# Optimization experiments

Measured on AMD Instinct MI355X. Metric: run time of the kernel, lower is better.

Reference implementation:

```python
import jax, jax.numpy as jnp
import numpy as np

N = 50000       # nodes
E = 800000      # edges (before self-loops)
F_IN = 128
HID = 64
HEADS = 4
OUT_DIM = 128
N_CLS = 2
NG = 500        # num graphs
SLOPE = 0.2     # GATConv leaky_relu negative slope
EPS = 1e-5      # BatchNorm eps


def setup_inputs() -> dict:
    key = jax.random.key(0)
    ks = jax.random.split(key, 24)
    s = 0.05
    d = {
        "x": jax.random.normal(ks[0], (N, F_IN), jnp.float32),
        "edge_index": jax.random.randint(ks[1], (2, E), 0, N, jnp.int64),
        "batch": jnp.sort(jax.random.randint(ks[2], (N,), 0, NG, jnp.int64)),
        # GATConv 1
        "W1": jax.random.normal(ks[3], (F_IN, HEADS * HID), jnp.float32) * s,
        "att_src1": jax.random.normal(ks[4], (HEADS, HID), jnp.float32) * s,
        "att_dst1": jax.random.normal(ks[5], (HEADS, HID), jnp.float32) * s,
        "b1": jnp.zeros((HEADS * HID,), jnp.float32),
        # BN1 (eval mode)
        "g1": jnp.ones((HEADS * HID,), jnp.float32),
        "be1": jnp.zeros((HEADS * HID,), jnp.float32),
        "rm1": jnp.zeros((HEADS * HID,), jnp.float32),
        "rv1": jnp.ones((HEADS * HID,), jnp.float32),
        # GATConv 2
        "W2": jax.random.normal(ks[6], (HEADS * HID, HEADS * HID), jnp.float32) * s,
        "att_src2": jax.random.normal(ks[7], (HEADS, HID), jnp.float32) * s,
        "att_dst2": jax.random.normal(ks[8], (HEADS, HID), jnp.float32) * s,
        "b2": jnp.zeros((HEADS * HID,), jnp.float32),
        # BN2 (eval mode)
        "g2": jnp.ones((HEADS * HID,), jnp.float32),
        "be2": jnp.zeros((HEADS * HID,), jnp.float32),
        "rm2": jnp.zeros((HEADS * HID,), jnp.float32),
        "rv2": jnp.ones((HEADS * HID,), jnp.float32),
        # MLP head
        "lw1": jax.random.normal(ks[9], (HEADS * HID, OUT_DIM), jnp.float32) * s,
        "lb1": jnp.zeros((OUT_DIM,), jnp.float32),
        "lw2": jax.random.normal(ks[10], (OUT_DIM, N_CLS), jnp.float32) * s,
        "lb2": jnp.zeros((N_CLS,), jnp.float32),
    }
    return d


def _gat_conv(x, src, dst, W, a_src, a_dst, b):
    """PyG GATConv (concat heads, add_self_loops=True, eval -> no dropout)."""
    n = x.shape[0]
    h = (x @ W).reshape(n, HEADS, -1)            # [N, H, C]
    loop = jnp.arange(n)
    s = jnp.concatenate([src, loop])             # self-loops appended
    d = jnp.concatenate([dst, loop])
    a_s = jnp.sum(h * a_src, axis=-1)            # [N, H]
    a_d = jnp.sum(h * a_dst, axis=-1)            # [N, H]
    e = jax.nn.leaky_relu(a_s[s] + a_d[d], SLOPE)   # [Et, H]
    # softmax over incoming edges per destination node
    m = jax.ops.segment_max(e, d, num_segments=n)
    ex = jnp.exp(e - m[d])
    denom = jax.ops.segment_sum(ex, d, num_segments=n)
    alpha = ex / denom[d]                        # [Et, H]
    msg = h[s] * alpha[:, :, None]               # [Et, H, C]
    out = jax.ops.segment_sum(msg, d, num_segments=n)
    return out.reshape(n, -1) + b


def _bn_eval(x, g, be, rm, rv):
    return (x - rm) * jax.lax.rsqrt(rv + EPS) * g + be


def reference(x, edge_index, batch, W1, att_src1, att_dst1, b1, g1, be1, rm1, rv1,
              W2, att_src2, att_dst2, b2, g2, be2, rm2, rv2, lw1, lb1, lw2, lb2):
    src, dst = edge_index[0], edge_index[1]
    h = jax.nn.relu(_gat_conv(x, src, dst, W1, att_src1, att_dst1, b1))
    h = _bn_eval(h, g1, be1, rm1, rv1)
    h = jax.nn.relu(_gat_conv(h, src, dst, W2, att_src2, att_dst2, b2))
    h = _bn_eval(h, g2, be2, rm2, rv2)
    # global mean pool over graphs
    sums = jax.ops.segment_sum(h, batch, num_segments=NG)
    cnt = jax.ops.segment_sum(jnp.ones((h.shape[0],), h.dtype), batch, num_segments=NG)
    pooled = sums / jnp.clip(cnt, 1.0)[:, None]
    z = jax.nn.relu(pooled @ lw1 + lb1)
    return z @ lw2 + lb2
```

## Files before the change

### kernel.cpp

```cpp
#include <hip/hip_runtime.h>
#include <hip/hip_bf16.h>
#include <math.h>

#define N_NODES 50000
#define M_PAD   50048
#define N_EDGES 800000
#define F_IN 128
#define HID 64
#define HEADS 4
#define FEAT 256
#define OUT_DIM 128
#define N_CLS 2
#define NG 500
#define SLOPE 0.2f
#define BN_EPS 1e-5f
#define ECAP 64
#define ET (N_EDGES + N_NODES)
#define EQ ((ET + 3) / 4)

typedef __attribute__((ext_vector_type(8))) short short8;
typedef __attribute__((ext_vector_type(4))) float floatx4;
typedef __attribute__((ext_vector_type(2))) float floatx2;

__device__ inline unsigned short f2bf(float f) {
    unsigned int u = __float_as_uint(f);
    unsigned int lsb = (u >> 16) & 1u;
    return (unsigned short)((u + 0x7fffu + lsb) >> 16);
}

template<bool AF32>
__global__ __launch_bounds__(256, 2) void gemm_mfma_gat(
    const void* __restrict__ Av, const unsigned short* __restrict__ BT,
    const float* __restrict__ att_src, const float* __restrict__ att_dst,
    unsigned char* __restrict__ h8, float* __restrict__ a_s,
    float* __restrict__ a_d, int K) {
    constexpr int LS = 40;
    constexpr int C8 = 272;
    __shared__ __align__(16) unsigned char smem_raw[128 * C8];
    unsigned short* As = (unsigned short*)smem_raw;
    unsigned short* Bs = As + 128 * LS;
    unsigned char*  s8 = smem_raw;
    int t = threadIdx.x;
    int lane = t & 63, w = t >> 6;
    int row0 = blockIdx.x * 128;
    int mrow = lane & 15, quad = lane >> 4;

    floatx4 acc[8][4] = {};

    int rA = t >> 2, cA = (t & 3) * 8;

    const unsigned short* Ab = (const unsigned short*)Av;
    const float* Af = (const float*)Av;

    for (int k0 = 0; k0 < K; k0 += 32) {
        #pragma unroll
        for (int j = 0; j < 2; j++) {
            int r = rA + j * 64;
            if (AF32) {
                uint4 pk = make_uint4(0, 0, 0, 0);
                if (row0 + r < N_NODES) {
                    float4 f0 = *(const float4*)&Af[(long long)(row0 + r) * K + k0 + cA];
                    float4 f1 = *(const float4*)&Af[(long long)(row0 + r) * K + k0 + cA + 4];
                    pk.x = (unsigned)f2bf(f0.x) | ((unsigned)f2bf(f0.y) << 16);
                    pk.y = (unsigned)f2bf(f0.z) | ((unsigned)f2bf(f0.w) << 16);
                    pk.z = (unsigned)f2bf(f1.x) | ((unsigned)f2bf(f1.y) << 16);
                    pk.w = (unsigned)f2bf(f1.z) | ((unsigned)f2bf(f1.w) << 16);
                }
                *(uint4*)&As[r * LS + cA] = pk;
            } else {
                *(uint4*)&As[r * LS + cA] = *(const uint4*)&Ab[(long long)(row0 + r) * K + k0 + cA];
            }
        }
        #pragma unroll
        for (int j = 0; j < 4; j++) {
            int r = rA + j * 64;
            *(uint4*)&Bs[r * LS + cA] = *(const uint4*)&BT[(long long)r * K + k0 + cA];
        }
        __syncthreads();
        short8 bf[4];
        #pragma unroll
        for (int ni = 0; ni < 4; ni++)
            bf[ni] = *(const short8*)&Bs[(w * 64 + ni * 16 + mrow) * LS + quad * 8];
        #pragma unroll
        for (int mi = 0; mi < 8; mi++) {
            short8 af = *(const short8*)&As[(mi * 16 + mrow) * LS + quad * 8];
            #pragma unroll
            for (int ni = 0; ni < 4; ni++)
                acc[mi][ni] = __builtin_amdgcn_mfma_f32_16x16x32_bf16(af, bf[ni],
                                                                      acc[mi][ni], 0, 0, 0);
        }
        __syncthreads();
    }

    float ats[4], atd[4];
    #pragma unroll
    for (int ni = 0; ni < 4; ni++) {
        ats[ni] = att_src[w * 64 + ni * 16 + mrow];
        atd[ni] = att_dst[w * 64 + ni * 16 + mrow];
    }
    #pragma unroll
    for (int mi = 0; mi < 8; mi++) {
        #pragma unroll
        for (int r = 0; r < 4; r++) {
            int row = row0 + mi * 16 + quad * 4 + r;
            float ps = 0.f, pd = 0.f;
            #pragma unroll
            for (int ni = 0; ni < 4; ni++) {
                float v = acc[mi][ni][r];
                ps += v * ats[ni];
                pd += v * atd[ni];
            }
            #pragma unroll
            for (int off = 1; off < 16; off <<= 1) {
                ps += __shfl_xor(ps, off);
                pd += __shfl_xor(pd, off);
            }
            if (mrow == 0 && row < N_NODES) {
                a_s[row * 4 + w] = ps;
                a_d[row * 4 + w] = pd;
            }
        }
    }

    #pragma unroll
    for (int mi = 0; mi < 8; mi++)
        #pragma unroll
        for (int r = 0; r < 4; r++) {
            int row = mi * 16 + quad * 4 + r;
            #pragma unroll
            for (int ni = 0; ni < 4; ni += 2) {
                int pk = __builtin_amdgcn_cvt_pk_fp8_f32(acc[mi][ni][r],
                                                         acc[mi][ni + 1][r], 0, false);
                s8[row * C8 + w * 64 + ni * 16 + mrow]       = (unsigned char)(pk & 0xff);
                s8[row * C8 + w * 64 + (ni + 1) * 16 + mrow] = (unsigned char)((pk >> 8) & 0xff);
            }
        }
    __syncthreads();
    {
        int r2 = t >> 1, half = t & 1;
        const uint4* sp = (const uint4*)&s8[r2 * C8 + half * 128];
        uint4* dp = (uint4*)&h8[(long long)(row0 + r2) * FEAT + half * 128];
        #pragma unroll
        for (int k = 0; k < 8; k++)
            dp[k] = sp[k];
    }
}

__global__ void prep(const float* __restrict__ W1, const float* __restrict__ W2,
                     unsigned short* __restrict__ W1T, unsigned short* __restrict__ W2T,
                     int* __restrict__ deg, int* __restrict__ ovf_cnt,
                     unsigned long long* __restrict__ h1bf_pad) {
    int i = blockIdx.x * 256 + threadIdx.x;
    if (i < F_IN * 256) {
        int k = i >> 8, n = i & 255;
        W1T[n * F_IN + k] = f2bf(W1[i]);
    }
    int j = i - F_IN * 256;
    if (j >= 0 && j < FEAT * 256) {
        int k = j >> 8, n = j & 255;
        W2T[n * FEAT + k] = f2bf(W2[j]);
    }
    if (i < N_NODES) deg[i] = 0;
    if (i == 0) *ovf_cnt = 0;
    if (i < (M_PAD - N_NODES) * FEAT / 4) h1bf_pad[i] = 0ULL;
}

__global__ __launch_bounds__(256) void build_ell(
    const int* __restrict__ src, const int* __restrict__ dst,
    int* __restrict__ deg, int* __restrict__ ell,
    int* __restrict__ ovf_cnt, int* __restrict__ ovf) {
    int i = blockIdx.x * 256 + threadIdx.x;
    if (i >= EQ) return;
    int ee[4], ss[4], dd[4], pp[4];
    int nv = 0;
    #pragma unroll
    for (int j = 0; j < 4; j++) {
        int e = i + j * EQ;
        if (e < ET) {
            ee[nv] = e;
            if (e < N_EDGES) { ss[nv] = src[e]; dd[nv] = dst[e]; }
            else             { ss[nv] = dd[nv] = e - N_EDGES; }
            nv++;
        }
    }
    #pragma unroll
    for (int j = 0; j < 4; j++)
        if (j < nv) pp[j] = atomicAdd(&deg[dd[j]], 1);
    #pragma unroll
    for (int j = 0; j < 4; j++) {
        if (j >= nv) continue;
        if (pp[j] < ECAP) {
            ell[dd[j] * ECAP + pp[j]] = ss[j];
        } else {
            int k = atomicAdd(ovf_cnt, 1);
            ovf[2 * k] = ss[j];
            ovf[2 * k + 1] = dd[j];
        }
    }
}

__global__ __launch_bounds__(256) void gat_fused(
    const int* __restrict__ deg_arr, const int* __restrict__ ell,
    const int* __restrict__ ovf_cnt, const int* __restrict__ ovf,
    const float* __restrict__ a_s, const float* __restrict__ a_d,
    const unsigned char* __restrict__ h8, const float* __restrict__ bias,
    const float* __restrict__ g, const float* __restrict__ be,
    const float* __restrict__ rm, const float* __restrict__ rv,
    unsigned short* __restrict__ out16) {
    int t = threadIdx.x;
    int lane = t & 63;
    int w = t >> 6;
    int hd = lane >> 4;
    int d = blockIdx.x * 4 + w;

    __shared__ float p_lds[4 * ECAP * 4];
    __shared__ int   o_lds[4 * ECAP];
    float* pw = &p_lds[w * ECAP * 4];
    int*   ow = &o_lds[w * ECAP];

    const unsigned int* __restrict__ H1 = (const unsigned int*)h8;

    int deg = deg_arr[d];
    float4 ad4 = *(const float4*)&a_d[d * 4];

    float den = 0.f;
    float4 acc = make_float4(0.f, 0.f, 0.f, 0.f);

    if (deg <= ECAP) {
        float lg[4] = {-INFINITY, -INFINITY, -INFINITY, -INFINITY};
        if (lane < deg) {
            int s = ell[d * ECAP + lane];
            ow[lane] = s * 64;
            float4 as4 = *(const float4*)&a_s[s * 4];
            float e0 = as4.x + ad4.x; lg[0] = e0 > 0.f ? e0 : SLOPE * e0;
            float e1 = as4.y + ad4.y; lg[1] = e1 > 0.f ? e1 : SLOPE * e1;
            float e2 = as4.z + ad4.z; lg[2] = e2 > 0.f ? e2 : SLOPE * e2;
            float e3 = as4.w + ad4.w; lg[3] = e3 > 0.f ? e3 : SLOPE * e3;
        }
        float mm = fmaxf(fmaxf(lg[0], lg[1]), fmaxf(lg[2], lg[3]));
        #pragma unroll
        for (int off = 1; off < 64; off <<= 1) mm = fmaxf(mm, __shfl_xor(mm, off));
        if (lane < deg) {
            float4 pq;
            pq.x = __expf(lg[0] - mm);
            pq.y = __expf(lg[1] - mm);
            pq.z = __expf(lg[2] - mm);
            pq.w = __expf(lg[3] - mm);
            *(float4*)&pw[lane * 4] = pq;
        }
        int e = 0;
        for (; e + 1 < deg; e += 2) {
            int oA = ow[e], oB = ow[e + 1];
            float pA = pw[e * 4 + hd], pB = pw[(e + 1) * 4 + hd];
            int uA = (int)H1[oA + lane];
            int uB = (int)H1[oB + lane];
            den += pA + pB;
            floatx2 a0 = __builtin_amdgcn_cvt_pk_f32_fp8(uA, false);
            floatx2 a1 = __builtin_amdgcn_cvt_pk_f32_fp8(uA, true);
            floatx2 b0 = __builtin_amdgcn_cvt_pk_f32_fp8(uB, false);
            floatx2 b1 = __builtin_amdgcn_cvt_pk_f32_fp8(uB, true);
            acc.x += pA * a0.x; acc.y += pA * a0.y;
            acc.z += pA * a1.x; acc.w += pA * a1.y;
            acc.x += pB * b0.x; acc.y += pB * b0.y;
            acc.z += pB * b1.x; acc.w += pB * b1.y;
        }
        if (e < deg) {
            int oA = ow[e];
            float pA = pw[e * 4 + hd];
            int uA = (int)H1[oA + lane];
            den += pA;
            floatx2 a0 = __builtin_amdgcn_cvt_pk_f32_fp8(uA, false);
            floatx2 a1 = __builtin_amdgcn_cvt_pk_f32_fp8(uA, true);
            acc.x += pA * a0.x; acc.y += pA * a0.y;
            acc.z += pA * a1.x; acc.w += pA * a1.y;
        }
    } else {
        float m_old;
        {
            int s = ell[d * ECAP + lane];
            ow[lane] = s * 64;
            float4 as4 = *(const float4*)&a_s[s * 4];
            float lg[4];
            float e0 = as4.x + ad4.x; lg[0] = e0 > 0.f ? e0 : SLOPE * e0;
            float e1 = as4.y + ad4.y; lg[1] = e1 > 0.f ? e1 : SLOPE * e1;
            float e2 = as4.z + ad4.z; lg[2] = e2 > 0.f ? e2 : SLOPE * e2;
            float e3 = as4.w + ad4.w; lg[3] = e3 > 0.f ? e3 : SLOPE * e3;
            float mm = fmaxf(fmaxf(lg[0], lg[1]), fmaxf(lg[2], lg[3]));
            #pragma unroll
            for (int off = 1; off < 64; off <<= 1) mm = fmaxf(mm, __shfl_xor(mm, off));
            m_old = mm;
            float4 pq;
            pq.x = __expf(lg[0] - mm);
            pq.y = __expf(lg[1] - mm);
            pq.z = __expf(lg[2] - mm);
            pq.w = __expf(lg[3] - mm);
            *(float4*)&pw[lane * 4] = pq;
            for (int e = 0; e < ECAP; e++) {
                int oA = ow[e];
                float pA = pw[e * 4 + hd];
                int uA = (int)H1[oA + lane];
                den += pA;
                floatx2 a0 = __builtin_amdgcn_cvt_pk_f32_fp8(uA, false);
                floatx2 a1 = __builtin_amdgcn_cvt_pk_f32_fp8(uA, true);
                acc.x += pA * a0.x; acc.y += pA * a0.y;
                acc.z += pA * a1.x; acc.w += pA * a1.y;
            }
        }
        int nov = *ovf_cnt;
        for (int i = 0; i < nov; i++) {
            int s2 = ovf[2 * i], d2 = ovf[2 * i + 1];
            if (d2 != d) continue;
            float4 as4 = *(const float4*)&a_s[s2 * 4];
            float lg[4];
            float e0 = as4.x + ad4.x; lg[0] = e0 > 0.f ? e0 : SLOPE * e0;
            float e1 = as4.y + ad4.y; lg[1] = e1 > 0.f ? e1 : SLOPE * e1;
            float e2 = as4.z + ad4.z; lg[2] = e2 > 0.f ? e2 : SLOPE * e2;
            float e3 = as4.w + ad4.w; lg[3] = e3 > 0.f ? e3 : SLOPE * e3;
            float mmax = fmaxf(fmaxf(lg[0], lg[1]), fmaxf(lg[2], lg[3]));
            float m_new = fmaxf(m_old, mmax);
            float alpha = __expf(m_old - m_new);
            m_old = m_new;
            float ph = __expf(lg[hd] - m_new);
            acc.x *= alpha; acc.y *= alpha; acc.z *= alpha; acc.w *= alpha;
            den = den * alpha + ph;
            int u = (int)H1[s2 * 64 + lane];
            floatx2 a0 = __builtin_amdgcn_cvt_pk_f32_fp8(u, false);
            floatx2 a1 = __builtin_amdgcn_cvt_pk_f32_fp8(u, true);
            acc.x += ph * a0.x; acc.y += ph * a0.y;
            acc.z += ph * a1.x; acc.w += ph * a1.y;
        }
    }
    float inv = 1.f / den;
    int c0 = lane * 4;
    float4 bi = *(const float4*)&bias[c0];
    float4 gg = *(const float4*)&g[c0];
    float4 bb = *(const float4*)&be[c0];
    float4 mm4 = *(const float4*)&rm[c0];
    float4 vv = *(const float4*)&rv[c0];
    float v0 = fmaxf(acc.x * inv + bi.x, 0.f);
    float v1 = fmaxf(acc.y * inv + bi.y, 0.f);
    float v2 = fmaxf(acc.z * inv + bi.z, 0.f);
    float v3 = fmaxf(acc.w * inv + bi.w, 0.f);
    v0 = (v0 - mm4.x) * rsqrtf(vv.x + BN_EPS) * gg.x + bb.x;
    v1 = (v1 - mm4.y) * rsqrtf(vv.y + BN_EPS) * gg.y + bb.y;
    v2 = (v2 - mm4.z) * rsqrtf(vv.z + BN_EPS) * gg.z + bb.z;
    v3 = (v3 - mm4.w) * rsqrtf(vv.w + BN_EPS) * gg.w + bb.w;
    unsigned long long o =
        (unsigned long long)f2bf(v0) |
        ((unsigned long long)f2bf(v1) << 16) |
        ((unsigned long long)f2bf(v2) << 32) |
        ((unsigned long long)f2bf(v3) << 48);
    __builtin_nontemporal_store(o, (unsigned long long*)&out16[(long long)d * FEAT + c0]);
}

__global__ __launch_bounds__(256) void head_fused(
    const unsigned short* __restrict__ h2, const int* __restrict__ batch,
    const float* __restrict__ lw1, const float* __restrict__ lb1,
    const float* __restrict__ lw2, const float* __restrict__ lb2,
    float* __restrict__ out) {
    int gph = blockIdx.x;
    int t = threadIdx.x;
    __shared__ float pooled[FEAT];
    __shared__ float zl[OUT_DIM];
    __shared__ int lo_s, hi_s;
    if (t == 0) {
        int lo = 0, hi = N_NODES;
        while (lo < hi) { int mid = (lo + hi) >> 1; if (batch[mid] < gph) lo = mid + 1; else hi = mid; }
        lo_s = lo;
        int lo2 = 0, hi2 = N_NODES;
        while (lo2 < hi2) { int mid = (lo2 + hi2) >> 1; if (batch[mid] < gph + 1) lo2 = mid + 1; else hi2 = mid; }
        hi_s = lo2;
    }
    __syncthreads();
    int lo = lo_s, hi = hi_s;
    float a0 = 0.f, a1 = 0.f, a2 = 0.f, a3 = 0.f;
    int n = lo;
    for (; n + 3 < hi; n += 4) {
        a0 += __uint_as_float((unsigned)h2[(long long)n * FEAT + t] << 16);
        a1 += __uint_as_float((unsigned)h2[(long long)(n + 1) * FEAT + t] << 16);
        a2 += __uint_as_float((unsigned)h2[(long long)(n + 2) * FEAT + t] << 16);
        a3 += __uint_as_float((unsigned)h2[(long long)(n + 3) * FEAT + t] << 16);
    }
    for (; n < hi; n++) a0 += __uint_as_float((unsigned)h2[(long long)n * FEAT + t] << 16);
    float cnt = fmaxf((float)(hi - lo), 1.f);
    pooled[t] = (a0 + a1 + a2 + a3) / cnt;
    __syncthreads();
    int j = t >> 1, kh = t & 1;
    float zp = 0.f;
    #pragma unroll 8
    for (int k = kh * 128; k < kh * 128 + 128; k++)
        zp += pooled[k] * lw1[k * OUT_DIM + j];
    zp += __shfl_xor(zp, 1);
    if (kh == 0) zl[j] = fmaxf(zp + lb1[j], 0.f);
    __syncthreads();
    int w = t >> 6, lane = t & 63;
    if (w < 2) {
        float p = zl[lane] * lw2[lane * 2 + w] + zl[lane + 64] * lw2[(lane + 64) * 2 + w];
        #pragma unroll
        for (int off = 1; off < 64; off <<= 1) p += __shfl_xor(p, off);
        if (lane == 0) out[gph * 2 + w] = p + lb2[w];
    }
}

extern "C" void kernel_launch(void* const* d_in, const int* in_sizes, int n_in,
                              void* d_out, int out_size, void* d_ws, size_t ws_size,
                              hipStream_t stream) {
    const float* x       = (const float*)d_in[0];
    const int*   ei      = (const int*)d_in[1];
    const int*   batch   = (const int*)d_in[2];
    const float* W1      = (const float*)d_in[3];
    const float* att_s1  = (const float*)d_in[4];
    const float* att_d1  = (const float*)d_in[5];
    const float* b1      = (const float*)d_in[6];
    const float* g1      = (const float*)d_in[7];
    const float* be1     = (const float*)d_in[8];
    const float* rm1     = (const float*)d_in[9];
    const float* rv1     = (const float*)d_in[10];
    const float* W2      = (const float*)d_in[11];
    const float* att_s2  = (const float*)d_in[12];
    const float* att_d2  = (const float*)d_in[13];
    const float* b2      = (const float*)d_in[14];
    const float* g2      = (const float*)d_in[15];
    const float* be2     = (const float*)d_in[16];
    const float* rm2     = (const float*)d_in[17];
    const float* rv2     = (const float*)d_in[18];
    const float* lw1     = (const float*)d_in[19];
    const float* lb1     = (const float*)d_in[20];
    const float* lw2     = (const float*)d_in[21];
    const float* lb2     = (const float*)d_in[22];
    float* out           = (float*)d_out;

    const int* src = ei;
    const int* dst = ei + N_EDGES;

    char* p = (char*)d_ws;
    auto carve = [&p](size_t bytes) -> void* {
        void* r = (void*)p;
        p += (bytes + 63) & ~(size_t)63;
        return r;
    };
    unsigned short* h2bf = (unsigned short*)carve(sizeof(short) * (size_t)N_NODES * FEAT);
    float* a_s    = (float*)carve(sizeof(float) * N_NODES * HEADS);
    float* a_d    = (float*)carve(sizeof(float) * N_NODES * HEADS);
    int*   deg    = (int*)carve(sizeof(int) * N_NODES);
    int*   ell    = (int*)carve(sizeof(int) * (size_t)N_NODES * ECAP);
    int*   ovf_cnt= (int*)carve(sizeof(int) * 16);
    int*   ovf    = (int*)carve(sizeof(int) * 2 * ET);
    unsigned char*  h8   = (unsigned char*)carve((size_t)M_PAD * FEAT);
    unsigned short* h1bf = (unsigned short*)carve(sizeof(short) * (size_t)M_PAD * FEAT);
    unsigned short* w1t  = (unsigned short*)carve(sizeof(short) * FEAT * F_IN);
    unsigned short* w2t  = (unsigned short*)carve(sizeof(short) * FEAT * FEAT);

    prep<<<((F_IN + FEAT) * 256 + 255) / 256, 256, 0, stream>>>(
        W1, W2, w1t, w2t, deg, ovf_cnt,
        (unsigned long long*)(h1bf + (size_t)N_NODES * FEAT));

    build_ell<<<(EQ + 255) / 256, 256, 0, stream>>>(src, dst, deg, ell, ovf_cnt, ovf);

    gemm_mfma_gat<true><<<M_PAD / 128, 256, 0, stream>>>(x, w1t, att_s1, att_d1,
                                                         h8, a_s, a_d, F_IN);
    gat_fused<<<N_NODES / 4, 256, 0, stream>>>(deg, ell, ovf_cnt, ovf, a_s, a_d, h8,
                                               b1, g1, be1, rm1, rv1, h1bf);

    gemm_mfma_gat<false><<<M_PAD / 128, 256, 0, stream>>>(h1bf, w2t, att_s2, att_d2,
                                                          h8, a_s, a_d, FEAT);
    gat_fused<<<N_NODES / 4, 256, 0, stream>>>(deg, ell, ovf_cnt, ovf, a_s, a_d, h8,
                                               b2, g2, be2, rm2, rv2, h2bf);

    head_fused<<<NG, 256, 0, stream>>>(h2bf, batch, lw1, lb1, lw2, lb2, out);
}
```

Before: 312.8 us.

## Fuse ELL adjacency build into first GEMM launch as extra blocks

Removes the separate build_ell kernel and appends its work as extra thread blocks to the first projection GEMM launch, so the atomic-heavy adjacency construction can run alongside the MFMA GEMM blocks. Each build thread now handles 2 edges instead of 4, which doubles the number of build blocks. This saves one kernel launch and its serialization gap. The build blocks still allocate the GEMM's large static shared memory, which may limit how many of them are resident at once.

```diff
diff --git a/kernel.cpp b/kernel.cpp
--- a/kernel.cpp
+++ b/kernel.cpp
@@ -4,6 +4,7 @@
 
 #define N_NODES 50000
 #define M_PAD   50048
+#define NBLK_GEMM (M_PAD / 128)
 #define N_EDGES 800000
 #define F_IN 128
 #define HID 64
@@ -16,7 +17,8 @@
 #define BN_EPS 1e-5f
 #define ECAP 64
 #define ET (N_EDGES + N_NODES)
-#define EQ ((ET + 3) / 4)
+#define EH ((ET + 1) / 2)
+#define NBLK_BUILD ((EH + 255) / 256)
 
 typedef __attribute__((ext_vector_type(8))) short short8;
 typedef __attribute__((ext_vector_type(4))) float floatx4;
@@ -28,19 +30,54 @@
     return (unsigned short)((u + 0x7fffu + lsb) >> 16);
 }
 
-template<bool AF32>
+template<bool AF32, bool BUILD>
 __global__ __launch_bounds__(256, 2) void gemm_mfma_gat(
     const void* __restrict__ Av, const unsigned short* __restrict__ BT,
     const float* __restrict__ att_src, const float* __restrict__ att_dst,
     unsigned char* __restrict__ h8, float* __restrict__ a_s,
-    float* __restrict__ a_d, int K) {
+    float* __restrict__ a_d, int K,
+    const int* __restrict__ src, const int* __restrict__ dst,
+    int* __restrict__ deg, int* __restrict__ ell,
+    int* __restrict__ ovf_cnt, int* __restrict__ ovf) {
     constexpr int LS = 40;
     constexpr int C8 = 272;
     __shared__ __align__(16) unsigned char smem_raw[128 * C8];
+    int t = threadIdx.x;
+
+    if (BUILD && blockIdx.x >= NBLK_GEMM) {
+        int i = (blockIdx.x - NBLK_GEMM) * 256 + t;
+        if (i >= EH) return;
+        int ss[2], dd[2], pp[2];
+        int nv = 0;
+        #pragma unroll
+        for (int j = 0; j < 2; j++) {
+            int e = i + j * EH;
+            if (e < ET) {
+                if (e < N_EDGES) { ss[nv] = src[e]; dd[nv] = dst[e]; }
+                else             { ss[nv] = dd[nv] = e - N_EDGES; }
+                nv++;
+            }
+        }
+        #pragma unroll
+        for (int j = 0; j < 2; j++)
+            if (j < nv) pp[j] = atomicAdd(&deg[dd[j]], 1);
+        #pragma unroll
+        for (int j = 0; j < 2; j++) {
+            if (j >= nv) continue;
+            if (pp[j] < ECAP) {
+                ell[dd[j] * ECAP + pp[j]] = ss[j];
+            } else {
+                int k = atomicAdd(ovf_cnt, 1);
+                ovf[2 * k] = ss[j];
+                ovf[2 * k + 1] = dd[j];
+            }
+        }
+        return;
+    }
+
     unsigned short* As = (unsigned short*)smem_raw;
     unsigned short* Bs = As + 128 * LS;
     unsigned char*  s8 = smem_raw;
-    int t = threadIdx.x;
     int lane = t & 63, w = t >> 6;
     int row0 = blockIdx.x * 128;
     int mrow = lane & 15, quad = lane >> 4;
@@ -163,40 +200,6 @@
     if (i < N_NODES) deg[i] = 0;
     if (i == 0) *ovf_cnt = 0;
     if (i < (M_PAD - N_NODES) * FEAT / 4) h1bf_pad[i] = 0ULL;
-}
-
-__global__ __launch_bounds__(256) void build_ell(
-    const int* __restrict__ src, const int* __restrict__ dst,
-    int* __restrict__ deg, int* __restrict__ ell,
-    int* __restrict__ ovf_cnt, int* __restrict__ ovf) {
-    int i = blockIdx.x * 256 + threadIdx.x;
-    if (i >= EQ) return;
-    int ee[4], ss[4], dd[4], pp[4];
-    int nv = 0;
-    #pragma unroll
-    for (int j = 0; j < 4; j++) {
-        int e = i + j * EQ;
-        if (e < ET) {
-            ee[nv] = e;
-            if (e < N_EDGES) { ss[nv] = src[e]; dd[nv] = dst[e]; }
-            else             { ss[nv] = dd[nv] = e - N_EDGES; }
-            nv++;
-        }
-    }
-    #pragma unroll
-    for (int j = 0; j < 4; j++)
-        if (j < nv) pp[j] = atomicAdd(&deg[dd[j]], 1);
-    #pragma unroll
-    for (int j = 0; j < 4; j++) {
-        if (j >= nv) continue;
-        if (pp[j] < ECAP) {
-            ell[dd[j] * ECAP + pp[j]] = ss[j];
-        } else {
-            int k = atomicAdd(ovf_cnt, 1);
-            ovf[2 * k] = ss[j];
-            ovf[2 * k + 1] = dd[j];
-        }
-    }
 }
 
 __global__ __launch_bounds__(256) void gat_fused(
@@ -455,15 +458,15 @@
         W1, W2, w1t, w2t, deg, ovf_cnt,
         (unsigned long long*)(h1bf + (size_t)N_NODES * FEAT));
 
-    build_ell<<<(EQ + 255) / 256, 256, 0, stream>>>(src, dst, deg, ell, ovf_cnt, ovf);
-
-    gemm_mfma_gat<true><<<M_PAD / 128, 256, 0, stream>>>(x, w1t, att_s1, att_d1,
-                                                         h8, a_s, a_d, F_IN);
+    gemm_mfma_gat<true, true><<<NBLK_GEMM + NBLK_BUILD, 256, 0, stream>>>(
+        x, w1t, att_s1, att_d1, h8, a_s, a_d, F_IN,
+        src, dst, deg, ell, ovf_cnt, ovf);
     gat_fused<<<N_NODES / 4, 256, 0, stream>>>(deg, ell, ovf_cnt, ovf, a_s, a_d, h8,
                                                b1, g1, be1, rm1, rv1, h1bf);
 
-    gemm_mfma_gat<false><<<M_PAD / 128, 256, 0, stream>>>(h1bf, w2t, att_s2, att_d2,
-                                                          h8, a_s, a_d, FEAT);
+    gemm_mfma_gat<false, false><<<NBLK_GEMM, 256, 0, stream>>>(
+        h1bf, w2t, att_s2, att_d2, h8, a_s, a_d, FEAT,
+        nullptr, nullptr, nullptr, nullptr, nullptr, nullptr);
     gat_fused<<<N_NODES / 4, 256, 0, stream>>>(deg, ell, ovf_cnt, ovf, a_s, a_d, h8,
                                                b2, g2, be2, rm2, rv2, h2bf);
 
```

Measured after the change: 307.4 us (median of 2 runs). Within noise of the previous version (-1.7%).
